# Kernel tuning notes

Hardware: AMD Instinct MI355X
Metric: run time of the kernel (lower is better)

## Reference

```python
import jax, jax.numpy as jnp
import numpy as np

DIM = 768
HEADS = 12
DIM_HEAD = 64
INNER = HEADS * DIM_HEAD  # 768
EPS = 1e-5


def setup_inputs() -> dict:
    key = jax.random.key(0)
    ks = jax.random.split(key, 5)
    x = jax.random.normal(ks[0], (4, 2048, DIM), dtype=jnp.float32)
    ln_g = jnp.ones((DIM,), dtype=jnp.float32)
    ln_b = jnp.zeros((DIM,), dtype=jnp.float32)
    s1 = 1.0 / np.sqrt(DIM)
    W_qkv = jax.random.uniform(ks[1], (DIM, 3 * INNER), dtype=jnp.float32, minval=-s1, maxval=s1)
    b_qkv = jax.random.uniform(ks[2], (3 * INNER,), dtype=jnp.float32, minval=-s1, maxval=s1)
    s2 = 1.0 / np.sqrt(INNER)
    W_out = jax.random.uniform(ks[3], (INNER, DIM), dtype=jnp.float32, minval=-s2, maxval=s2)
    b_out = jax.random.uniform(ks[4], (DIM,), dtype=jnp.float32, minval=-s2, maxval=s2)
    return {"x": x, "ln_g": ln_g, "ln_b": ln_b, "W_qkv": W_qkv, "b_qkv": b_qkv, "W_out": W_out, "b_out": b_out}


def reference(x, ln_g, ln_b, W_qkv, b_qkv, W_out, b_out):
    b, n, _ = x.shape
    # pre-norm LayerNorm
    mu = jnp.mean(x, axis=-1, keepdims=True)
    var = jnp.mean(jnp.square(x - mu), axis=-1, keepdims=True)
    xn = (x - mu) * jax.lax.rsqrt(var + EPS) * ln_g + ln_b
    qkv = xn @ W_qkv + b_qkv  # [b, n, 3*inner]
    q, k, v = jnp.split(qkv, 3, axis=-1)
    def to_heads(t):
        return t.reshape(b, n, HEADS, DIM_HEAD).transpose(0, 2, 1, 3)  # b h n d
    q, k, v = map(to_heads, (q, k, v))
    q = q * (DIM_HEAD ** -0.5)
    sim = jnp.einsum('bhid,bhjd->bhij', q, k)
    attn = jax.nn.softmax(sim, axis=-1)  # dropout is identity (p=0.0)
    out = jnp.einsum('bhij,bhjd->bhid', attn, v)
    out = out.transpose(0, 2, 1, 3).reshape(b, n, INNER)
    return out @ W_out + b_out
```

## Files before the change

kernel.cpp:

```cpp
#include <hip/hip_runtime.h>
#include <cstdint>
#include <cstddef>


#define SEQ    2048
#define NBATCH 4
#define DMODEL 768
#define NHEADS 12
#define DHEAD  64
#define MROWS  (NBATCH * SEQ)
#define NQKV   (3 * DMODEL)
#define KT     64
#define NT     (SEQ / KT)

using f32x4  = __attribute__((ext_vector_type(4))) float;
using u16x8  = __attribute__((ext_vector_type(8))) unsigned short;
using s16x8  = __attribute__((ext_vector_type(8))) short;

__device__ __forceinline__ unsigned short f2bf(float f) {
  union { float f; unsigned int u; } x; x.f = f;
  unsigned int r = x.u + 0x7fffu + ((x.u >> 16) & 1u);
  return (unsigned short)(r >> 16);
}

#if defined(__has_builtin)
#if __has_builtin(__builtin_amdgcn_cvt_pk_bf16_f32)
#define HAVE_PK_BF16 1
#endif
#endif
__device__ __forceinline__ unsigned int pk_bf16(float a, float b) {
#ifdef HAVE_PK_BF16
  auto v = __builtin_amdgcn_cvt_pk_bf16_f32(a, b);
  union { decltype(v) v2; unsigned int u; } c; c.v2 = v; return c.u;
#else
  return (unsigned int)f2bf(a) | ((unsigned int)f2bf(b) << 16);
#endif
}

__device__ __forceinline__ f32x4 mfma16(u16x8 a, u16x8 b, f32x4 c) {
  return __builtin_amdgcn_mfma_f32_16x16x32_bf16((s16x8)a, (s16x8)b, c, 0, 0, 0);
}

__device__ __forceinline__ void gl_lds16(const void* g, void* l) {
  __builtin_amdgcn_global_load_lds(
      (const __attribute__((address_space(1))) void*)g,
      (__attribute__((address_space(3))) void*)l, 16, 0, 0);
}

__global__ __launch_bounds__(256) void ln_kernel(
    const float* __restrict__ x, const float* __restrict__ g,
    const float* __restrict__ bb, unsigned short* __restrict__ xn) {
  __shared__ float red[8];
  const int row = blockIdx.x, t = threadIdx.x;
  const float* xr = x + (size_t)row * DMODEL;
  float v0 = xr[t], v1 = xr[t + 256], v2 = xr[t + 512];
  float s = v0 + v1 + v2;
#pragma unroll
  for (int o = 32; o; o >>= 1) s += __shfl_down(s, o);
  if ((t & 63) == 0) red[t >> 6] = s;
  __syncthreads();
  float mu = (red[0] + red[1] + red[2] + red[3]) * (1.0f / DMODEL);
  float d0 = v0 - mu, d1 = v1 - mu, d2 = v2 - mu;
  float q = d0 * d0 + d1 * d1 + d2 * d2;
#pragma unroll
  for (int o = 32; o; o >>= 1) q += __shfl_down(q, o);
  if ((t & 63) == 0) red[4 + (t >> 6)] = q;
  __syncthreads();
  float var = (red[4] + red[5] + red[6] + red[7]) * (1.0f / DMODEL);
  float rstd = rsqrtf(var + 1e-5f);
  size_t base = (size_t)row * DMODEL;
  xn[base + t]       = f2bf(d0 * rstd * g[t]       + bb[t]);
  xn[base + t + 256] = f2bf(d1 * rstd * g[t + 256] + bb[t + 256]);
  xn[base + t + 512] = f2bf(d2 * rstd * g[t + 512] + bb[t + 512]);
}

__global__ __launch_bounds__(256) void tconv_kernel(
    const float* __restrict__ W, unsigned short* __restrict__ Wt, int N) {
  __shared__ float tile[32][33];
  const int n0 = blockIdx.x * 32, k0 = blockIdx.y * 32;
  const int tx = threadIdx.x & 31, ty = threadIdx.x >> 5;
#pragma unroll
  for (int r = 0; r < 4; ++r)
    tile[ty + r * 8][tx] = W[(size_t)(k0 + ty + r * 8) * N + n0 + tx];
  __syncthreads();
#pragma unroll
  for (int r = 0; r < 4; ++r)
    Wt[(size_t)(n0 + ty + r * 8) * DMODEL + k0 + tx] = f2bf(tile[tx][ty + r * 8]);
}

__global__ __launch_bounds__(256, 3) void gemm_qkv_kernel(
    const unsigned short* __restrict__ A, const unsigned short* __restrict__ Bt,
    const float* __restrict__ bias, unsigned short* __restrict__ qb,
    unsigned short* __restrict__ kb, unsigned short* __restrict__ vt) {
  __shared__ alignas(16) unsigned short As[128 * 64];
  __shared__ alignas(16) unsigned short Bs[128 * 64];
  const int t = threadIdx.x, wid = t >> 6, l = t & 63, quad = l >> 4, ll = l & 15;
  const int m0 = blockIdx.x * 128, n0 = blockIdx.y * 128;
  const int wm = (wid >> 1) * 64, wn = (wid & 1) * 64;
  const int srow = l >> 3;
  const int sblk = (l & 7) ^ srow;
  f32x4 acc[4][4] = {};
  for (int k0 = 0; k0 < DMODEL; k0 += 64) {
#pragma unroll
    for (int cc = 0; cc < 4; ++cc) {
      int call = wid * 4 + cc;
      int r = call * 8 + srow;
      gl_lds16(A  + (size_t)(m0 + r) * DMODEL + k0 + sblk * 8, &As[call * 512]);
      gl_lds16(Bt + (size_t)(n0 + r) * DMODEL + k0 + sblk * 8, &Bs[call * 512]);
    }
    __syncthreads();
#pragma unroll
    for (int ks = 0; ks < 2; ++ks) {
      u16x8 af[4], bf[4];
#pragma unroll
      for (int i = 0; i < 4; ++i) {
        int ra = wm + i * 16 + ll, rb = wn + i * 16 + ll;
        int blk = (ks * 4 + quad) ^ (ll & 7);
        af[i] = *(const u16x8*)&As[ra * 64 + blk * 8];
        bf[i] = *(const u16x8*)&Bs[rb * 64 + blk * 8];
      }
#pragma unroll
      for (int mi = 0; mi < 4; ++mi)
#pragma unroll
        for (int ni = 0; ni < 4; ++ni)
          acc[mi][ni] = mfma16(af[mi], bf[ni], acc[mi][ni]);
    }
    __syncthreads();
  }
  const int which = (n0 >= 2 * DMODEL) ? 2 : (n0 >= DMODEL ? 1 : 0);
#pragma unroll
  for (int mi = 0; mi < 4; ++mi) {
    int gm = m0 + wm + mi * 16 + quad * 4;
    int b = gm >> 11, i0 = gm & 2047;
#pragma unroll
    for (int ni = 0; ni < 4; ++ni) {
      int gn = n0 + wn + ni * 16 + ll;
      float bv = bias[gn];
      int rem = gn - which * DMODEL;
      int h = rem >> 6, d = rem & 63;
      int bh = b * NHEADS + h;
      if (which == 0) {
#pragma unroll
        for (int r = 0; r < 4; ++r)
          qb[(size_t)(bh * SEQ + i0 + r) * DHEAD + d] = f2bf((acc[mi][ni][r] + bv) * 0.125f);
      } else if (which == 1) {
#pragma unroll
        for (int r = 0; r < 4; ++r)
          kb[(size_t)(bh * SEQ + i0 + r) * DHEAD + d] = f2bf(acc[mi][ni][r] + bv);
      } else {
        uint2 pk;
        pk.x = pk_bf16(acc[mi][ni][0] + bv, acc[mi][ni][1] + bv);
        pk.y = pk_bf16(acc[mi][ni][2] + bv, acc[mi][ni][3] + bv);
        *(uint2*)&vt[((size_t)bh * DHEAD + d) * SEQ + i0] = pk;
      }
    }
  }
}

__global__ __launch_bounds__(256, 3) void attn_kernel(
    const unsigned short* __restrict__ qbuf, const unsigned short* __restrict__ kbuf,
    const unsigned short* __restrict__ vtg, unsigned short* __restrict__ ao) {
  __shared__ alignas(16) unsigned short stage[2][2][KT * DHEAD];
  __shared__ alignas(16) unsigned short Pws[4][32 * 72];
  const int t = threadIdx.x, wid = t >> 6, l = t & 63, quad = l >> 4, ll = l & 15;
  const int qt = blockIdx.x, bh = blockIdx.y;
  const unsigned short* qg  = qbuf + ((size_t)bh * SEQ + qt * 128) * DHEAD;
  const unsigned short* kg0 = kbuf + (size_t)bh * SEQ * DHEAD;
  const unsigned short* vt0 = vtg  + (size_t)bh * DHEAD * SEQ;
  const int srow = l >> 3;
  const int sblk = (l & 7) ^ srow;

  unsigned short* Qs = &stage[0][0][0];
#pragma unroll
  for (int cc = 0; cc < 4; ++cc) {
    int call = wid * 4 + cc;
    gl_lds16(qg + (call * 8 + srow) * 64 + sblk * 8, Qs + call * 512);
  }
  __syncthreads();
  u16x8 qf[2][2];
#pragma unroll
  for (int mi = 0; mi < 2; ++mi)
#pragma unroll
    for (int ks = 0; ks < 2; ++ks) {
      int r = wid * 32 + mi * 16 + ll;
      int blk = (ks * 4 + quad) ^ (ll & 7);
      qf[mi][ks] = *(const u16x8*)&Qs[r * 64 + blk * 8];
    }
  __syncthreads();

  auto stage_tile = [&](int buf, int kt2) {
    const unsigned short* kg = kg0 + (size_t)kt2 * KT * DHEAD;
#pragma unroll
    for (int c = 0; c < 2; ++c) {
      int call = wid * 2 + c;
      int r = call * 8 + srow;
      gl_lds16(kg + r * 64 + sblk * 8, &stage[buf][0][call * 512]);
      gl_lds16(vt0 + (size_t)r * SEQ + kt2 * KT + sblk * 8, &stage[buf][1][call * 512]);
    }
  };

  f32x4 oacc[2][4] = {};
  float lsum[2] = {0.f, 0.f};
  unsigned short* Pw = Pws[wid];

  stage_tile(0, 0);
  int buf = 0;
  for (int kt2 = 0; kt2 < NT; ++kt2) {
    __syncthreads();
    if (kt2 + 1 < NT) stage_tile(buf ^ 1, kt2 + 1);
    const unsigned short* Ks = &stage[buf][0][0];
    const unsigned short* Vs = &stage[buf][1][0];

    f32x4 st[2][4] = {};
#pragma unroll
    for (int ks = 0; ks < 2; ++ks)
#pragma unroll
      for (int ni = 0; ni < 4; ++ni) {
        int r = ni * 16 + ll;
        int blk = (ks * 4 + quad) ^ (ll & 7);
        u16x8 kf = *(const u16x8*)&Ks[r * 64 + blk * 8];
        st[0][ni] = mfma16(kf, qf[0][ks], st[0][ni]);
        st[1][ni] = mfma16(kf, qf[1][ks], st[1][ni]);
      }

#pragma unroll
    for (int mi = 0; mi < 2; ++mi)
#pragma unroll
      for (int ni = 0; ni < 4; ++ni) {
        float p0 = __expf(st[mi][ni][0]);
        float p1 = __expf(st[mi][ni][1]);
        float p2 = __expf(st[mi][ni][2]);
        float p3 = __expf(st[mi][ni][3]);
        lsum[mi] += (p0 + p1) + (p2 + p3);
        uint2 pk;
        pk.x = pk_bf16(p0, p1);
        pk.y = pk_bf16(p2, p3);
        *(uint2*)&Pw[(mi * 16 + ll) * 72 + ni * 16 + quad * 4] = pk;
      }
    asm volatile("s_waitcnt lgkmcnt(0)" ::: "memory");

#pragma unroll
    for (int ks = 0; ks < 2; ++ks) {
      u16x8 pf0 = *(const u16x8*)&Pw[(ll) * 72 + ks * 32 + quad * 8];
      u16x8 pf1 = *(const u16x8*)&Pw[(16 + ll) * 72 + ks * 32 + quad * 8];
#pragma unroll
      for (int di = 0; di < 4; ++di) {
        int r = di * 16 + ll;
        int blk = (ks * 4 + quad) ^ (ll & 7);
        u16x8 vf = *(const u16x8*)&Vs[r * 64 + blk * 8];
        oacc[0][di] = mfma16(pf0, vf, oacc[0][di]);
        oacc[1][di] = mfma16(pf1, vf, oacc[1][di]);
      }
    }
    buf ^= 1;
  }

  float lsF[2];
#pragma unroll
  for (int mi = 0; mi < 2; ++mi) {
    float ls = lsum[mi];
    ls += __shfl_xor(ls, 16);
    ls += __shfl_xor(ls, 32);
    lsF[mi] = ls;
  }

  const int b = bh / NHEADS, h = bh - b * NHEADS;
#pragma unroll
  for (int mi = 0; mi < 2; ++mi) {
#pragma unroll
    for (int r = 0; r < 4; ++r) {
      float inv = 1.0f / __shfl(lsF[mi], quad * 4 + r);
      int row = qt * 128 + wid * 32 + mi * 16 + quad * 4 + r;
      size_t base = ((size_t)(b * SEQ + row)) * DMODEL + h * DHEAD;
#pragma unroll
      for (int di = 0; di < 4; ++di)
        ao[base + di * 16 + ll] = f2bf(oacc[mi][di][r] * inv);
    }
  }
}

__global__ __launch_bounds__(256, 3) void gemm_out_kernel(
    const unsigned short* __restrict__ A, const unsigned short* __restrict__ Bt,
    const float* __restrict__ bias, float* __restrict__ out) {
  __shared__ alignas(16) unsigned short As[128 * 64];
  __shared__ alignas(16) unsigned short Bs[128 * 64];
  const int t = threadIdx.x, wid = t >> 6, l = t & 63, quad = l >> 4, ll = l & 15;
  const int m0 = blockIdx.x * 128, n0 = blockIdx.y * 128;
  const int wm = (wid >> 1) * 64, wn = (wid & 1) * 64;
  const int srow = l >> 3;
  const int sblk = (l & 7) ^ srow;
  f32x4 acc[4][4] = {};
  for (int k0 = 0; k0 < DMODEL; k0 += 64) {
#pragma unroll
    for (int cc = 0; cc < 4; ++cc) {
      int call = wid * 4 + cc;
      int r = call * 8 + srow;
      gl_lds16(A  + (size_t)(m0 + r) * DMODEL + k0 + sblk * 8, &As[call * 512]);
      gl_lds16(Bt + (size_t)(n0 + r) * DMODEL + k0 + sblk * 8, &Bs[call * 512]);
    }
    __syncthreads();
#pragma unroll
    for (int ks = 0; ks < 2; ++ks) {
      u16x8 af[4], bf[4];
#pragma unroll
      for (int i = 0; i < 4; ++i) {
        int ra = wm + i * 16 + ll, rb = wn + i * 16 + ll;
        int blk = (ks * 4 + quad) ^ (ll & 7);
        af[i] = *(const u16x8*)&As[ra * 64 + blk * 8];
        bf[i] = *(const u16x8*)&Bs[rb * 64 + blk * 8];
      }
#pragma unroll
      for (int mi = 0; mi < 4; ++mi)
#pragma unroll
        for (int ni = 0; ni < 4; ++ni)
          acc[mi][ni] = mfma16(af[mi], bf[ni], acc[mi][ni]);
    }
    __syncthreads();
  }
#pragma unroll
  for (int mi = 0; mi < 4; ++mi) {
#pragma unroll
    for (int ni = 0; ni < 4; ++ni) {
      int gm = m0 + wm + mi * 16 + quad * 4;
      int gn = n0 + wn + ni * 16 + ll;
      float bv = bias[gn];
#pragma unroll
      for (int r = 0; r < 4; ++r)
        out[(size_t)(gm + r) * DMODEL + gn] = acc[mi][ni][r] + bv;
    }
  }
}

extern "C" void kernel_launch(void* const* d_in, const int* in_sizes, int n_in,
                              void* d_out, int out_size, void* d_ws, size_t ws_size,
                              hipStream_t stream) {
  const float* x     = (const float*)d_in[0];
  const float* ln_g  = (const float*)d_in[1];
  const float* ln_b  = (const float*)d_in[2];
  const float* W_qkv = (const float*)d_in[3];
  const float* b_qkv = (const float*)d_in[4];
  const float* W_out = (const float*)d_in[5];
  const float* b_out = (const float*)d_in[6];
  float* out = (float*)d_out;

  char* ws = (char*)d_ws;
  unsigned short* xn    = (unsigned short*)(ws);
  unsigned short* wqkvt = (unsigned short*)(ws + 12582912);
  unsigned short* woutt = (unsigned short*)(ws + 16121856);
  unsigned short* qb    = (unsigned short*)(ws + 17301504);
  unsigned short* kb    = (unsigned short*)(ws + 29884416);
  unsigned short* vt    = (unsigned short*)(ws + 42467328);
  unsigned short* ao    = xn;

  ln_kernel<<<MROWS, 256, 0, stream>>>(x, ln_g, ln_b, xn);
  tconv_kernel<<<dim3(NQKV / 32, DMODEL / 32), 256, 0, stream>>>(W_qkv, wqkvt, NQKV);
  tconv_kernel<<<dim3(DMODEL / 32, DMODEL / 32), 256, 0, stream>>>(W_out, woutt, DMODEL);
  gemm_qkv_kernel<<<dim3(MROWS / 128, NQKV / 128), 256, 0, stream>>>(xn, wqkvt, b_qkv, qb, kb, vt);
  attn_kernel<<<dim3(SEQ / 128, NBATCH * NHEADS), 256, 0, stream>>>(qb, kb, vt, ao);
  gemm_out_kernel<<<dim3(MROWS / 128, DMODEL / 128), 256, 0, stream>>>(ao, woutt, b_out, out);
}
```

Baseline: 244.5 us.

## Swap GEMM operand roles for vectorized epilogue stores and use exp2 softmax

Splits the QKV GEMM into a Q/K kernel and a separate V kernel. The Q/K kernel computes the transposed product (weights as the M side) so each lane writes four contiguous head-dim values as one packed 8-byte store instead of scattered 2-byte stores. The output GEMM is transposed the same way so results go out as float4 stores, with a float4 bias load. Q is pre-scaled by log2(e)/8 so attention can use the hardware exp2 in place of __expf. Launch bounds drop from 3 to 2 blocks per CU, which may lower occupancy, and the extra launch adds a little overhead.

```diff
diff --git a/kernel.cpp b/kernel.cpp
--- a/kernel.cpp
+++ b/kernel.cpp
@@ -27,13 +27,25 @@
 #if __has_builtin(__builtin_amdgcn_cvt_pk_bf16_f32)
 #define HAVE_PK_BF16 1
 #endif
+#if __has_builtin(__builtin_amdgcn_exp2f)
+#define HAVE_EXP2 1
 #endif
+#endif
+
 __device__ __forceinline__ unsigned int pk_bf16(float a, float b) {
 #ifdef HAVE_PK_BF16
   auto v = __builtin_amdgcn_cvt_pk_bf16_f32(a, b);
   union { decltype(v) v2; unsigned int u; } c; c.v2 = v; return c.u;
 #else
   return (unsigned int)f2bf(a) | ((unsigned int)f2bf(b) << 16);
+#endif
+}
+
+__device__ __forceinline__ float fexp2(float x) {
+#ifdef HAVE_EXP2
+  return __builtin_amdgcn_exp2f(x);
+#else
+  return exp2f(x);
 #endif
 }
 
@@ -88,17 +100,76 @@
     Wt[(size_t)(n0 + ty + r * 8) * DMODEL + k0 + tx] = f2bf(tile[tx][ty + r * 8]);
 }
 
-__global__ __launch_bounds__(256, 3) void gemm_qkv_kernel(
-    const unsigned short* __restrict__ A, const unsigned short* __restrict__ Bt,
+__global__ __launch_bounds__(256, 2) void gemm_qk_kernel(
+    const unsigned short* __restrict__ Wt, const unsigned short* __restrict__ xn,
     const float* __restrict__ bias, unsigned short* __restrict__ qb,
-    unsigned short* __restrict__ kb, unsigned short* __restrict__ vt) {
+    unsigned short* __restrict__ kb) {
   __shared__ alignas(16) unsigned short As[128 * 64];
   __shared__ alignas(16) unsigned short Bs[128 * 64];
   const int t = threadIdx.x, wid = t >> 6, l = t & 63, quad = l >> 4, ll = l & 15;
-  const int m0 = blockIdx.x * 128, n0 = blockIdx.y * 128;
+  const int a0 = blockIdx.x * 128;
+  const int b0 = blockIdx.y * 128;
+  const int wa = (wid >> 1) * 64, wb = (wid & 1) * 64;
+  const int srow = l >> 3, sblk = (l & 7) ^ srow;
+  f32x4 acc[4][4] = {};
+  for (int k0 = 0; k0 < DMODEL; k0 += 64) {
+#pragma unroll
+    for (int cc = 0; cc < 4; ++cc) {
+      int call = wid * 4 + cc;
+      int r = call * 8 + srow;
+      gl_lds16(Wt + (size_t)(a0 + r) * DMODEL + k0 + sblk * 8, &As[call * 512]);
+      gl_lds16(xn + (size_t)(b0 + r) * DMODEL + k0 + sblk * 8, &Bs[call * 512]);
+    }
+    __syncthreads();
+#pragma unroll
+    for (int ks = 0; ks < 2; ++ks) {
+      u16x8 af[4], bf[4];
+#pragma unroll
+      for (int i = 0; i < 4; ++i) {
+        int ra = wa + i * 16 + ll, rb = wb + i * 16 + ll;
+        int blk = (ks * 4 + quad) ^ (ll & 7);
+        af[i] = *(const u16x8*)&As[ra * 64 + blk * 8];
+        bf[i] = *(const u16x8*)&Bs[rb * 64 + blk * 8];
+      }
+#pragma unroll
+      for (int mi = 0; mi < 4; ++mi)
+#pragma unroll
+        for (int ni = 0; ni < 4; ++ni)
+          acc[mi][ni] = mfma16(af[mi], bf[ni], acc[mi][ni]);
+    }
+    __syncthreads();
+  }
+  const bool isq = (a0 < DMODEL);
+  unsigned short* dst = isq ? qb : kb;
+  const float sc = isq ? 0.18033688f : 1.0f;
+#pragma unroll
+  for (int mi = 0; mi < 4; ++mi) {
+    int row0 = a0 + wa + mi * 16 + quad * 4;
+    float4 bv = *(const float4*)&bias[row0];
+    int rr = isq ? row0 : row0 - DMODEL;
+    int h = rr >> 6, d0 = rr & 63;
+#pragma unroll
+    for (int ni = 0; ni < 4; ++ni) {
+      int seq = b0 + wb + ni * 16 + ll;
+      int b = seq >> 11, i = seq & 2047;
+      uint2 pk;
+      pk.x = pk_bf16((acc[mi][ni][0] + bv.x) * sc, (acc[mi][ni][1] + bv.y) * sc);
+      pk.y = pk_bf16((acc[mi][ni][2] + bv.z) * sc, (acc[mi][ni][3] + bv.w) * sc);
+      *(uint2*)&dst[(size_t)((b * NHEADS + h) * SEQ + i) * DHEAD + d0] = pk;
+    }
+  }
+}
+
+__global__ __launch_bounds__(256, 2) void gemm_v_kernel(
+    const unsigned short* __restrict__ A, const unsigned short* __restrict__ Bt,
+    const float* __restrict__ bias, unsigned short* __restrict__ vt) {
+  __shared__ alignas(16) unsigned short As[128 * 64];
+  __shared__ alignas(16) unsigned short Bs[128 * 64];
+  const int t = threadIdx.x, wid = t >> 6, l = t & 63, quad = l >> 4, ll = l & 15;
+  const int m0 = blockIdx.x * 128;
+  const int n0 = 2 * DMODEL + blockIdx.y * 128;
   const int wm = (wid >> 1) * 64, wn = (wid & 1) * 64;
-  const int srow = l >> 3;
-  const int sblk = (l & 7) ^ srow;
+  const int srow = l >> 3, sblk = (l & 7) ^ srow;
   f32x4 acc[4][4] = {};
   for (int k0 = 0; k0 < DMODEL; k0 += 64) {
 #pragma unroll
@@ -127,7 +198,6 @@
     }
     __syncthreads();
   }
-  const int which = (n0 >= 2 * DMODEL) ? 2 : (n0 >= DMODEL ? 1 : 0);
 #pragma unroll
   for (int mi = 0; mi < 4; ++mi) {
     int gm = m0 + wm + mi * 16 + quad * 4;
@@ -136,23 +206,13 @@
     for (int ni = 0; ni < 4; ++ni) {
       int gn = n0 + wn + ni * 16 + ll;
       float bv = bias[gn];
-      int rem = gn - which * DMODEL;
+      int rem = gn - 2 * DMODEL;
       int h = rem >> 6, d = rem & 63;
       int bh = b * NHEADS + h;
-      if (which == 0) {
-#pragma unroll
-        for (int r = 0; r < 4; ++r)
-          qb[(size_t)(bh * SEQ + i0 + r) * DHEAD + d] = f2bf((acc[mi][ni][r] + bv) * 0.125f);
-      } else if (which == 1) {
-#pragma unroll
-        for (int r = 0; r < 4; ++r)
-          kb[(size_t)(bh * SEQ + i0 + r) * DHEAD + d] = f2bf(acc[mi][ni][r] + bv);
-      } else {
-        uint2 pk;
-        pk.x = pk_bf16(acc[mi][ni][0] + bv, acc[mi][ni][1] + bv);
-        pk.y = pk_bf16(acc[mi][ni][2] + bv, acc[mi][ni][3] + bv);
-        *(uint2*)&vt[((size_t)bh * DHEAD + d) * SEQ + i0] = pk;
-      }
+      uint2 pk;
+      pk.x = pk_bf16(acc[mi][ni][0] + bv, acc[mi][ni][1] + bv);
+      pk.y = pk_bf16(acc[mi][ni][2] + bv, acc[mi][ni][3] + bv);
+      *(uint2*)&vt[((size_t)bh * DHEAD + d) * SEQ + i0] = pk;
     }
   }
 }
@@ -227,10 +287,10 @@
     for (int mi = 0; mi < 2; ++mi)
 #pragma unroll
       for (int ni = 0; ni < 4; ++ni) {
-        float p0 = __expf(st[mi][ni][0]);
-        float p1 = __expf(st[mi][ni][1]);
-        float p2 = __expf(st[mi][ni][2]);
-        float p3 = __expf(st[mi][ni][3]);
+        float p0 = fexp2(st[mi][ni][0]);
+        float p1 = fexp2(st[mi][ni][1]);
+        float p2 = fexp2(st[mi][ni][2]);
+        float p3 = fexp2(st[mi][ni][3]);
         lsum[mi] += (p0 + p1) + (p2 + p3);
         uint2 pk;
         pk.x = pk_bf16(p0, p1);
@@ -279,24 +339,24 @@
   }
 }
 
-__global__ __launch_bounds__(256, 3) void gemm_out_kernel(
-    const unsigned short* __restrict__ A, const unsigned short* __restrict__ Bt,
+__global__ __launch_bounds__(256, 2) void gemm_out_kernel(
+    const unsigned short* __restrict__ Wt, const unsigned short* __restrict__ ao,
     const float* __restrict__ bias, float* __restrict__ out) {
   __shared__ alignas(16) unsigned short As[128 * 64];
   __shared__ alignas(16) unsigned short Bs[128 * 64];
   const int t = threadIdx.x, wid = t >> 6, l = t & 63, quad = l >> 4, ll = l & 15;
-  const int m0 = blockIdx.x * 128, n0 = blockIdx.y * 128;
-  const int wm = (wid >> 1) * 64, wn = (wid & 1) * 64;
-  const int srow = l >> 3;
-  const int sblk = (l & 7) ^ srow;
+  const int a0 = blockIdx.x * 128;
+  const int b0 = blockIdx.y * 128;
+  const int wa = (wid >> 1) * 64, wb = (wid & 1) * 64;
+  const int srow = l >> 3, sblk = (l & 7) ^ srow;
   f32x4 acc[4][4] = {};
   for (int k0 = 0; k0 < DMODEL; k0 += 64) {
 #pragma unroll
     for (int cc = 0; cc < 4; ++cc) {
       int call = wid * 4 + cc;
       int r = call * 8 + srow;
-      gl_lds16(A  + (size_t)(m0 + r) * DMODEL + k0 + sblk * 8, &As[call * 512]);
-      gl_lds16(Bt + (size_t)(n0 + r) * DMODEL + k0 + sblk * 8, &Bs[call * 512]);
+      gl_lds16(Wt + (size_t)(a0 + r) * DMODEL + k0 + sblk * 8, &As[call * 512]);
+      gl_lds16(ao + (size_t)(b0 + r) * DMODEL + k0 + sblk * 8, &Bs[call * 512]);
     }
     __syncthreads();
 #pragma unroll
@@ -304,7 +364,7 @@
       u16x8 af[4], bf[4];
 #pragma unroll
       for (int i = 0; i < 4; ++i) {
-        int ra = wm + i * 16 + ll, rb = wn + i * 16 + ll;
+        int ra = wa + i * 16 + ll, rb = wb + i * 16 + ll;
         int blk = (ks * 4 + quad) ^ (ll & 7);
         af[i] = *(const u16x8*)&As[ra * 64 + blk * 8];
         bf[i] = *(const u16x8*)&Bs[rb * 64 + blk * 8];
@@ -319,14 +379,17 @@
   }
 #pragma unroll
   for (int mi = 0; mi < 4; ++mi) {
+    int row0 = a0 + wa + mi * 16 + quad * 4;
+    float4 bv = *(const float4*)&bias[row0];
 #pragma unroll
     for (int ni = 0; ni < 4; ++ni) {
-      int gm = m0 + wm + mi * 16 + quad * 4;
-      int gn = n0 + wn + ni * 16 + ll;
-      float bv = bias[gn];
-#pragma unroll
-      for (int r = 0; r < 4; ++r)
-        out[(size_t)(gm + r) * DMODEL + gn] = acc[mi][ni][r] + bv;
+      int seq = b0 + wb + ni * 16 + ll;
+      float4 o;
+      o.x = acc[mi][ni][0] + bv.x;
+      o.y = acc[mi][ni][1] + bv.y;
+      o.z = acc[mi][ni][2] + bv.z;
+      o.w = acc[mi][ni][3] + bv.w;
+      *(float4*)&out[(size_t)seq * DMODEL + row0] = o;
     }
   }
 }
@@ -355,7 +418,8 @@
   ln_kernel<<<MROWS, 256, 0, stream>>>(x, ln_g, ln_b, xn);
   tconv_kernel<<<dim3(NQKV / 32, DMODEL / 32), 256, 0, stream>>>(W_qkv, wqkvt, NQKV);
   tconv_kernel<<<dim3(DMODEL / 32, DMODEL / 32), 256, 0, stream>>>(W_out, woutt, DMODEL);
-  gemm_qkv_kernel<<<dim3(MROWS / 128, NQKV / 128), 256, 0, stream>>>(xn, wqkvt, b_qkv, qb, kb, vt);
+  gemm_qk_kernel<<<dim3(12, 64), 256, 0, stream>>>(wqkvt, xn, b_qkv, qb, kb);
+  gemm_v_kernel<<<dim3(64, 6), 256, 0, stream>>>(xn, wqkvt, b_qkv, vt);
   attn_kernel<<<dim3(SEQ / 128, NBATCH * NHEADS), 256, 0, stream>>>(qb, kb, vt, ao);
-  gemm_out_kernel<<<dim3(MROWS / 128, DMODEL / 128), 256, 0, stream>>>(ao, woutt, b_out, out);
-}
+  gemm_out_kernel<<<dim3(6, 64), 256, 0, stream>>>(woutt, ao, b_out, out);
+}
```

After: 240.2 us. Within noise of the previous version (-1.7%).
